# Kernel optimization log

Measured on AMD Instinct MI355X. Metric: run time of the kernel, lower is better.

Reference implementation:

```python
import jax, jax.numpy as jnp
import numpy as np

TEMPERATURE = 0.1

def setup_inputs() -> dict:
    key = jax.random.key(0)
    k1, k2 = jax.random.split(key)
    B, D = 8192, 512
    anchor = jax.random.normal(k1, (B, D), dtype=jnp.float32)
    positive = jax.random.normal(k2, (B, D), dtype=jnp.float32)
    return {"anchor": anchor, "positive": positive}

def reference(anchor, positive):
    # sim[i, j] = <anchor_i, positive_j> / T  -- [B, B]
    sim = jnp.einsum("bd,nd->bn", anchor, positive) / TEMPERATURE
    # InfoNCE with in-batch negatives: positive is the diagonal; since softmax
    # is permutation-invariant, -log_softmax(logits)[pos] = logsumexp(row) - diag.
    loss = jax.nn.logsumexp(sim, axis=1) - jnp.diagonal(sim)
    return jnp.mean(loss)
```

## Files before the change

### kernel.cpp

```cpp
#include <hip/hip_runtime.h>
#include <hip/hip_bf16.h>
#include <math.h>
#include <stdint.h>


#define NB 8192
#define DDIM 512
#define SPLITS 8
#define BM 256
#define BN 256
#define CPB (NB / SPLITS)
#define NROUND 32

#define DELTA 0.045f
#define INV_DELTA (1.0f / DELTA)
#define OUT_SCALE (DELTA * DELTA * 10.0f)
#define K2F (OUT_SCALE * 1.4426950408889634f)
#define LN2F 0.6931471805599453f

typedef unsigned char u8;
typedef __attribute__((ext_vector_type(4))) int i32x4;

__device__ __forceinline__ float fexp2(float x) {
#if __has_builtin(__builtin_amdgcn_exp2f)
  return __builtin_amdgcn_exp2f(x);
#else
  return __expf(x * LN2F);
#endif
}
__device__ __forceinline__ float flog2(float x) {
#if __has_builtin(__builtin_amdgcn_logf)
  return __builtin_amdgcn_logf(x);
#else
  return __logf(x) * 1.4426950408889634f;
#endif
}

__device__ __forceinline__ void gl2lds16(const u8* g, const u8* l) {
  __builtin_amdgcn_global_load_lds(
      (__attribute__((address_space(1))) unsigned int*)(uintptr_t)g,
      (__attribute__((address_space(3))) unsigned int*)(unsigned int)(uintptr_t)l,
      16, 0, 0);
}

__device__ __forceinline__ unsigned pack4(float x0, float x1, float x2, float x3) {
  int q0 = min(127, max(-127, __float2int_rn(x0 * INV_DELTA)));
  int q1 = min(127, max(-127, __float2int_rn(x1 * INV_DELTA)));
  int q2 = min(127, max(-127, __float2int_rn(x2 * INV_DELTA)));
  int q3 = min(127, max(-127, __float2int_rn(x3 * INV_DELTA)));
  return (q0 & 0xFF) | ((q1 & 0xFF) << 8) | ((q2 & 0xFF) << 16) | ((q3 & 0xFF) << 24);
}

__global__ void cvt_diag_kernel(const float* __restrict__ a, const float* __restrict__ p,
                                u8* __restrict__ aq, u8* __restrict__ pq,
                                float* __restrict__ diag, float* __restrict__ out) {
  if (blockIdx.x == 0 && threadIdx.x == 0) out[0] = 0.f;
  int row = (blockIdx.x * 256 + threadIdx.x) >> 6;
  int lane = threadIdx.x & 63;
  const float4* ar = (const float4*)(a + (size_t)row * DDIM + lane * 8);
  const float4* pr = (const float4*)(p + (size_t)row * DDIM + lane * 8);
  float4 a0 = ar[0], a1 = ar[1];
  float4 p0 = pr[0], p1 = pr[1];
  *(uint2*)(aq + (size_t)row * DDIM + lane * 8) =
      (uint2){pack4(a0.x, a0.y, a0.z, a0.w), pack4(a1.x, a1.y, a1.z, a1.w)};
  *(uint2*)(pq + (size_t)row * DDIM + lane * 8) =
      (uint2){pack4(p0.x, p0.y, p0.z, p0.w), pack4(p1.x, p1.y, p1.z, p1.w)};
  float s = a0.x * p0.x + a0.y * p0.y + a0.z * p0.z + a0.w * p0.w +
            a1.x * p1.x + a1.y * p1.y + a1.z * p1.z + a1.w * p1.w;
  for (int off = 32; off > 0; off >>= 1) s += __shfl_down(s, off);
  if (lane == 0) diag[row] = s * 10.0f;
}

__device__ __forceinline__ void fold_lse(i32x4 (&acc)[4][8], float (&rm)[4][4],
                                         float (&rl)[4][4]) {
#pragma unroll
  for (int mi = 0; mi < 4; ++mi) {
#pragma unroll
    for (int rr = 0; rr < 4; ++rr) {
      int im = acc[mi][0][rr];
#pragma unroll
      for (int ni = 1; ni < 8; ++ni) im = max(im, acc[mi][ni][rr]);
      const float mf = (float)im * K2F;
      const float nm = fmaxf(rm[mi][rr], mf);
      float add = 0.f;
#pragma unroll
      for (int ni = 0; ni < 8; ++ni)
        add += fexp2(fmaf((float)acc[mi][ni][rr], K2F, -nm));
      rl[mi][rr] = rl[mi][rr] * fexp2(rm[mi][rr] - nm) + add;
      rm[mi][rr] = nm;
#pragma unroll
      for (int ni = 0; ni < 8; ++ni) acc[mi][ni][rr] = 0;
    }
  }
}

__global__ __launch_bounds__(512, 2) void gemm_lse(
    const u8* __restrict__ Aq, const u8* __restrict__ Bq,
    float* __restrict__ partLse) {
  __shared__ u8 sA[4][BM * 64];
  __shared__ u8 sB[4][BN * 64];

  const int tid = threadIdx.x;
  const int wave = tid >> 6;
  const int lane = tid & 63;
  const int quad = lane >> 4;
  const int l16 = lane & 15;
  const int wr = wave >> 1;
  const int wc = wave & 1;

  const int bid = blockIdx.x;
  const int xcd = bid & 7;
  const int idx = bid >> 3;
  const int rowTile = (idx & 3) * 8 + xcd;
  const int colSplit = idx >> 2;
  const int row0 = rowTile * BM;
  const int col0 = colSplit * CPB;

  const int rsub = lane >> 2;
  const int qsrc = (lane & 3) ^ ((rsub >> 1) & 3);
  const u8* aCol = Aq + (size_t)(row0 + wave * 32 + rsub) * DDIM + qsrc * 16;
  const u8* bCol = Bq + (size_t)(col0 + wave * 32 + rsub) * DDIM + qsrc * 16;
  const int ldsOff = wave * 2048;

  const int sw = (l16 >> 1) & 3;
  const int fragA = (wr * 64 + l16) * 64 + ((quad ^ sw) * 16);
  const int fragB = (wc * 128 + l16) * 64 + ((quad ^ sw) * 16);

  i32x4 acc[4][8];
#pragma unroll
  for (int mi = 0; mi < 4; ++mi)
#pragma unroll
    for (int ni = 0; ni < 8; ++ni) acc[mi][ni] = (i32x4){0, 0, 0, 0};

  float rm[4][4], rl[4][4];
#pragma unroll
  for (int mi = 0; mi < 4; ++mi)
#pragma unroll
    for (int rr = 0; rr < 4; ++rr) { rm[mi][rr] = -INFINITY; rl[mi][rr] = 0.f; }

#define STAGE_A(t)                                                       \
  do {                                                                   \
    const int _kk = ((t) & 7) << 6, _bf = (t) & 3;                       \
    const u8* _a = aCol + _kk;                                           \
    gl2lds16(_a, &sA[_bf][ldsOff]);                                      \
    gl2lds16(_a + 16 * DDIM, &sA[_bf][ldsOff + 1024]);                   \
  } while (0)
#define STAGE_B(t)                                                       \
  do {                                                                   \
    const int _kk = ((t) & 7) << 6, _bf = (t) & 3;                       \
    const u8* _b = bCol + ((t) >> 3) * (BN * DDIM) + _kk;                \
    gl2lds16(_b, &sB[_bf][ldsOff]);                                      \
    gl2lds16(_b + 16 * DDIM, &sB[_bf][ldsOff + 1024]);                   \
  } while (0)

  STAGE_A(0); STAGE_B(0);
  STAGE_A(1); STAGE_B(1);
  STAGE_A(2); STAGE_B(2);
  asm volatile("s_waitcnt vmcnt(8)");
  __builtin_amdgcn_s_barrier();

#define MF8(AR, MI)                                                                 \
  acc[MI][0] = __builtin_amdgcn_mfma_i32_16x16x64_i8(AR, bq0, acc[MI][0], 0, 0, 0); \
  acc[MI][1] = __builtin_amdgcn_mfma_i32_16x16x64_i8(AR, bq1, acc[MI][1], 0, 0, 0); \
  acc[MI][2] = __builtin_amdgcn_mfma_i32_16x16x64_i8(AR, bq2, acc[MI][2], 0, 0, 0); \
  acc[MI][3] = __builtin_amdgcn_mfma_i32_16x16x64_i8(AR, bq3, acc[MI][3], 0, 0, 0); \
  acc[MI][4] = __builtin_amdgcn_mfma_i32_16x16x64_i8(AR, bq4, acc[MI][4], 0, 0, 0); \
  acc[MI][5] = __builtin_amdgcn_mfma_i32_16x16x64_i8(AR, bq5, acc[MI][5], 0, 0, 0); \
  acc[MI][6] = __builtin_amdgcn_mfma_i32_16x16x64_i8(AR, bq6, acc[MI][6], 0, 0, 0); \
  acc[MI][7] = __builtin_amdgcn_mfma_i32_16x16x64_i8(AR, bq7, acc[MI][7], 0, 0, 0);

#define ROUND_BODY(r, DO_STAGE)                                          \
  do {                                                                   \
    const int _b = (r) & 3;                                              \
    const u8* _sa = &sA[_b][0];                                          \
    const u8* _sb = &sB[_b][0];                                          \
    i32x4 bq0 = *(const i32x4*)(_sb + fragB + 0 * 1024);                 \
    i32x4 bq1 = *(const i32x4*)(_sb + fragB + 1 * 1024);                 \
    i32x4 bq2 = *(const i32x4*)(_sb + fragB + 2 * 1024);                 \
    i32x4 bq3 = *(const i32x4*)(_sb + fragB + 3 * 1024);                 \
    i32x4 bq4 = *(const i32x4*)(_sb + fragB + 4 * 1024);                 \
    i32x4 bq5 = *(const i32x4*)(_sb + fragB + 5 * 1024);                 \
    i32x4 bq6 = *(const i32x4*)(_sb + fragB + 6 * 1024);                 \
    i32x4 bq7 = *(const i32x4*)(_sb + fragB + 7 * 1024);                 \
    i32x4 a0 = *(const i32x4*)(_sa + fragA + 0 * 1024);                  \
    i32x4 a1 = *(const i32x4*)(_sa + fragA + 1 * 1024);                  \
    i32x4 a2 = *(const i32x4*)(_sa + fragA + 2 * 1024);                  \
    i32x4 a3 = *(const i32x4*)(_sa + fragA + 3 * 1024);                  \
    if (DO_STAGE) { STAGE_A((r) + 3); STAGE_B((r) + 3); }                \
    MF8(a0, 0) MF8(a1, 1) MF8(a2, 2) MF8(a3, 3)                          \
    if (((r) & 7) == 7) fold_lse(acc, rm, rl);                           \
  } while (0)

  for (int r = 0; r < NROUND - 3; ++r) {
    ROUND_BODY(r, 1);
    asm volatile("s_waitcnt vmcnt(8)");
    __builtin_amdgcn_s_barrier();
  }
  ROUND_BODY(NROUND - 3, 0);
  asm volatile("s_waitcnt vmcnt(4)");
  __builtin_amdgcn_s_barrier();
  ROUND_BODY(NROUND - 2, 0);
  asm volatile("s_waitcnt vmcnt(0)");
  __builtin_amdgcn_s_barrier();
  ROUND_BODY(NROUND - 1, 0);
  __builtin_amdgcn_s_barrier();
#undef ROUND_BODY
#undef MF8
#undef STAGE_A
#undef STAGE_B

  float2* const scr = (float2*)&sA[0][0];
#pragma unroll
  for (int mi = 0; mi < 4; ++mi) {
#pragma unroll
    for (int rr = 0; rr < 4; ++rr) {
      float m = rm[mi][rr], l = rl[mi][rr];
#pragma unroll
      for (int mask = 1; mask < 16; mask <<= 1) {
        float om = __shfl_xor(m, mask);
        float ol = __shfl_xor(l, mask);
        float nm = fmaxf(m, om);
        l = l * fexp2(m - nm) + ol * fexp2(om - nm);
        m = nm;
      }
      if (l16 == 0) {
        int rowl = wr * 64 + mi * 16 + quad * 4 + rr;
        scr[wc * 256 + rowl] = (float2){m, l};
      }
    }
  }
  __syncthreads();
  if (tid < BM) {
    float2 p0 = scr[tid], p1 = scr[256 + tid];
    float nm = fmaxf(p0.x, p1.x);
    float L = p0.y * fexp2(p0.x - nm) + p1.y * fexp2(p1.x - nm);
    partLse[(size_t)colSplit * NB + row0 + tid] = nm + flog2(L);
  }
}

__global__ void reduce_kernel(const float* __restrict__ partLse,
                              const float* __restrict__ diag, float* __restrict__ out) {
  __shared__ float red[4];
  int r = blockIdx.x * 256 + threadIdx.x;
  float M = -INFINITY;
#pragma unroll
  for (int s = 0; s < SPLITS; ++s) M = fmaxf(M, partLse[(size_t)s * NB + r]);
  float L = 0.f;
#pragma unroll
  for (int s = 0; s < SPLITS; ++s) L += fexp2(partLse[(size_t)s * NB + r] - M);
  float v = (M + flog2(L)) * LN2F - diag[r];
  for (int off = 32; off > 0; off >>= 1) v += __shfl_down(v, off);
  if ((threadIdx.x & 63) == 0) red[threadIdx.x >> 6] = v;
  __syncthreads();
  if (threadIdx.x == 0) {
    float s = (red[0] + red[1] + red[2] + red[3]) * (1.0f / (float)NB);
    atomicAdd(out, s);
  }
}

extern "C" void kernel_launch(void* const* d_in, const int* in_sizes, int n_in,
                              void* d_out, int out_size, void* d_ws, size_t ws_size,
                              hipStream_t stream) {
  const float* anchor = (const float*)d_in[0];
  const float* positive = (const float*)d_in[1];
  float* out = (float*)d_out;

  char* ws = (char*)d_ws;
  u8* Aq = (u8*)ws;
  u8* Bq = (u8*)(ws + (size_t)4194304);
  float* diag = (float*)(ws + (size_t)8388608);
  float* partLse = (float*)(ws + (size_t)8388608 + 32768);

  cvt_diag_kernel<<<NB / 4, 256, 0, stream>>>(anchor, positive, Aq, Bq, diag, out);
  gemm_lse<<<SPLITS * (NB / BM), 512, 0, stream>>>(Aq, Bq, partLse);
  reduce_kernel<<<NB / 256, 256, 0, stream>>>(partLse, diag, out);
}
```

Measured before the change: 117.2 us.

## Split each round into halves with register double-buffered LDS fragments and mid-round barrier

The int8 MFMA main loop is restructured. Each K-round now runs in two halves. The first half uses fragments preloaded in registers, then waits and passes the barrier, issues the global-to-LDS staging, and prefetches the next round's first fragments into an alternate register set before doing the second half of the MFMAs. All 32 rounds are unrolled, and s_setprio raises wave priority around the MFMA bursts. The aim is to hide LDS read latency and barrier stalls behind matrix work, at the cost of more registers and code size. The vmcnt accounting also changes, which risks ordering mistakes.

```diff
diff --git a/kernel.cpp b/kernel.cpp
--- a/kernel.cpp
+++ b/kernel.cpp
@@ -159,53 +159,81 @@
   asm volatile("s_waitcnt vmcnt(8)");
   __builtin_amdgcn_s_barrier();
 
-#define MF8(AR, MI)                                                                 \
-  acc[MI][0] = __builtin_amdgcn_mfma_i32_16x16x64_i8(AR, bq0, acc[MI][0], 0, 0, 0); \
-  acc[MI][1] = __builtin_amdgcn_mfma_i32_16x16x64_i8(AR, bq1, acc[MI][1], 0, 0, 0); \
-  acc[MI][2] = __builtin_amdgcn_mfma_i32_16x16x64_i8(AR, bq2, acc[MI][2], 0, 0, 0); \
-  acc[MI][3] = __builtin_amdgcn_mfma_i32_16x16x64_i8(AR, bq3, acc[MI][3], 0, 0, 0); \
-  acc[MI][4] = __builtin_amdgcn_mfma_i32_16x16x64_i8(AR, bq4, acc[MI][4], 0, 0, 0); \
-  acc[MI][5] = __builtin_amdgcn_mfma_i32_16x16x64_i8(AR, bq5, acc[MI][5], 0, 0, 0); \
-  acc[MI][6] = __builtin_amdgcn_mfma_i32_16x16x64_i8(AR, bq6, acc[MI][6], 0, 0, 0); \
-  acc[MI][7] = __builtin_amdgcn_mfma_i32_16x16x64_i8(AR, bq7, acc[MI][7], 0, 0, 0);
-
-#define ROUND_BODY(r, DO_STAGE)                                          \
-  do {                                                                   \
-    const int _b = (r) & 3;                                              \
-    const u8* _sa = &sA[_b][0];                                          \
-    const u8* _sb = &sB[_b][0];                                          \
-    i32x4 bq0 = *(const i32x4*)(_sb + fragB + 0 * 1024);                 \
-    i32x4 bq1 = *(const i32x4*)(_sb + fragB + 1 * 1024);                 \
-    i32x4 bq2 = *(const i32x4*)(_sb + fragB + 2 * 1024);                 \
-    i32x4 bq3 = *(const i32x4*)(_sb + fragB + 3 * 1024);                 \
-    i32x4 bq4 = *(const i32x4*)(_sb + fragB + 4 * 1024);                 \
-    i32x4 bq5 = *(const i32x4*)(_sb + fragB + 5 * 1024);                 \
-    i32x4 bq6 = *(const i32x4*)(_sb + fragB + 6 * 1024);                 \
-    i32x4 bq7 = *(const i32x4*)(_sb + fragB + 7 * 1024);                 \
-    i32x4 a0 = *(const i32x4*)(_sa + fragA + 0 * 1024);                  \
-    i32x4 a1 = *(const i32x4*)(_sa + fragA + 1 * 1024);                  \
-    i32x4 a2 = *(const i32x4*)(_sa + fragA + 2 * 1024);                  \
-    i32x4 a3 = *(const i32x4*)(_sa + fragA + 3 * 1024);                  \
-    if (DO_STAGE) { STAGE_A((r) + 3); STAGE_B((r) + 3); }                \
-    MF8(a0, 0) MF8(a1, 1) MF8(a2, 2) MF8(a3, 3)                          \
-    if (((r) & 7) == 7) fold_lse(acc, rm, rl);                           \
-  } while (0)
-
-  for (int r = 0; r < NROUND - 3; ++r) {
-    ROUND_BODY(r, 1);
-    asm volatile("s_waitcnt vmcnt(8)");
-    __builtin_amdgcn_s_barrier();
-  }
-  ROUND_BODY(NROUND - 3, 0);
-  asm volatile("s_waitcnt vmcnt(4)");
-  __builtin_amdgcn_s_barrier();
-  ROUND_BODY(NROUND - 2, 0);
-  asm volatile("s_waitcnt vmcnt(0)");
-  __builtin_amdgcn_s_barrier();
-  ROUND_BODY(NROUND - 1, 0);
-  __builtin_amdgcn_s_barrier();
-#undef ROUND_BODY
-#undef MF8
+  i32x4 xb0, xb1, xb2, xb3, xa0, xa1;
+  i32x4 yb0, yb1, yb2, yb3, ya0, ya1;
+  xb0 = *(const i32x4*)(&sB[0][fragB + 0 * 1024]);
+  xb1 = *(const i32x4*)(&sB[0][fragB + 1 * 1024]);
+  xb2 = *(const i32x4*)(&sB[0][fragB + 2 * 1024]);
+  xb3 = *(const i32x4*)(&sB[0][fragB + 3 * 1024]);
+  xa0 = *(const i32x4*)(&sA[0][fragA + 0 * 1024]);
+  xa1 = *(const i32x4*)(&sA[0][fragA + 1 * 1024]);
+
+#define VMW4 asm volatile("s_waitcnt vmcnt(4)")
+#define VMW0 asm volatile("s_waitcnt vmcnt(0)")
+
+#define MF4(AR, MI, B0, B1, B2, B3, NBASE)                                                    \
+  acc[MI][NBASE + 0] = __builtin_amdgcn_mfma_i32_16x16x64_i8(AR, B0, acc[MI][NBASE + 0], 0, 0, 0); \
+  acc[MI][NBASE + 1] = __builtin_amdgcn_mfma_i32_16x16x64_i8(AR, B1, acc[MI][NBASE + 1], 0, 0, 0); \
+  acc[MI][NBASE + 2] = __builtin_amdgcn_mfma_i32_16x16x64_i8(AR, B2, acc[MI][NBASE + 2], 0, 0, 0); \
+  acc[MI][NBASE + 3] = __builtin_amdgcn_mfma_i32_16x16x64_i8(AR, B3, acc[MI][NBASE + 3], 0, 0, 0);
+
+#define RND(r, CB0, CB1, CB2, CB3, CA0, CA1, NB0, NB1, NB2, NB3, NA0, NA1, \
+            DO_STAGE, VMSTMT, DO_PREF, DO_FOLD)                           \
+  {                                                                       \
+    const u8* _sa = &sA[(r) & 3][0];                                      \
+    const u8* _sb = &sB[(r) & 3][0];                                      \
+    i32x4 _a2 = *(const i32x4*)(_sa + fragA + 2 * 1024);                  \
+    i32x4 _a3 = *(const i32x4*)(_sa + fragA + 3 * 1024);                  \
+    i32x4 _b4 = *(const i32x4*)(_sb + fragB + 4 * 1024);                  \
+    i32x4 _b5 = *(const i32x4*)(_sb + fragB + 5 * 1024);                  \
+    i32x4 _b6 = *(const i32x4*)(_sb + fragB + 6 * 1024);                  \
+    i32x4 _b7 = *(const i32x4*)(_sb + fragB + 7 * 1024);                  \
+    __builtin_amdgcn_s_setprio(1);                                        \
+    MF4(CA0, 0, CB0, CB1, CB2, CB3, 0)                                    \
+    MF4(CA1, 1, CB0, CB1, CB2, CB3, 0)                                    \
+    MF4(_a2, 2, CB0, CB1, CB2, CB3, 0)                                    \
+    MF4(_a3, 3, CB0, CB1, CB2, CB3, 0)                                    \
+    __builtin_amdgcn_s_setprio(0);                                        \
+    VMSTMT;                                                               \
+    __builtin_amdgcn_s_barrier();                                         \
+    if (DO_STAGE) { STAGE_A((r) + 3); STAGE_B((r) + 3); }                 \
+    if (DO_PREF) {                                                        \
+      const u8* _na = &sA[((r) + 1) & 3][0];                              \
+      const u8* _nb = &sB[((r) + 1) & 3][0];                              \
+      NB0 = *(const i32x4*)(_nb + fragB + 0 * 1024);                      \
+      NB1 = *(const i32x4*)(_nb + fragB + 1 * 1024);                      \
+      NB2 = *(const i32x4*)(_nb + fragB + 2 * 1024);                      \
+      NB3 = *(const i32x4*)(_nb + fragB + 3 * 1024);                      \
+      NA0 = *(const i32x4*)(_na + fragA + 0 * 1024);                      \
+      NA1 = *(const i32x4*)(_na + fragA + 1 * 1024);                      \
+    }                                                                     \
+    __builtin_amdgcn_s_setprio(1);                                        \
+    MF4(CA0, 0, _b4, _b5, _b6, _b7, 4)                                    \
+    MF4(CA1, 1, _b4, _b5, _b6, _b7, 4)                                    \
+    MF4(_a2, 2, _b4, _b5, _b6, _b7, 4)                                    \
+    MF4(_a3, 3, _b4, _b5, _b6, _b7, 4)                                    \
+    __builtin_amdgcn_s_setprio(0);                                        \
+    if (DO_FOLD) fold_lse(acc, rm, rl);                                   \
+  }
+
+#define RX(r, DS, VM, PF, FL) RND(r, xb0, xb1, xb2, xb3, xa0, xa1, yb0, yb1, yb2, yb3, ya0, ya1, DS, VM, PF, FL)
+#define RY(r, DS, VM, PF, FL) RND(r, yb0, yb1, yb2, yb3, ya0, ya1, xb0, xb1, xb2, xb3, xa0, xa1, DS, VM, PF, FL)
+
+  RX(0, 1, VMW4, 1, 0)  RY(1, 1, VMW4, 1, 0)  RX(2, 1, VMW4, 1, 0)  RY(3, 1, VMW4, 1, 0)
+  RX(4, 1, VMW4, 1, 0)  RY(5, 1, VMW4, 1, 0)  RX(6, 1, VMW4, 1, 0)  RY(7, 1, VMW4, 1, 1)
+  RX(8, 1, VMW4, 1, 0)  RY(9, 1, VMW4, 1, 0)  RX(10, 1, VMW4, 1, 0) RY(11, 1, VMW4, 1, 0)
+  RX(12, 1, VMW4, 1, 0) RY(13, 1, VMW4, 1, 0) RX(14, 1, VMW4, 1, 0) RY(15, 1, VMW4, 1, 1)
+  RX(16, 1, VMW4, 1, 0) RY(17, 1, VMW4, 1, 0) RX(18, 1, VMW4, 1, 0) RY(19, 1, VMW4, 1, 0)
+  RX(20, 1, VMW4, 1, 0) RY(21, 1, VMW4, 1, 0) RX(22, 1, VMW4, 1, 0) RY(23, 1, VMW4, 1, 1)
+  RX(24, 1, VMW4, 1, 0) RY(25, 1, VMW4, 1, 0) RX(26, 1, VMW4, 1, 0) RY(27, 1, VMW4, 1, 0)
+  RX(28, 1, VMW4, 1, 0) RY(29, 0, VMW4, 1, 0) RX(30, 0, VMW0, 1, 0) RY(31, 0, (void)0, 0, 1)
+
+#undef RX
+#undef RY
+#undef RND
+#undef MF4
+#undef VMW4
+#undef VMW0
 #undef STAGE_A
 #undef STAGE_B
 
```

New measurement: 245.0 us. 2.09x slower.

## Split GEMM tile across 16 waves with 64x64 per-wave subtiles

Applied to the files above, without the earlier changes.

Doubles the workgroup to 1024 threads, arranging 16 waves in a 4x4 grid so each wave computes a 64x64 sub-tile instead of 64x128. Staging, wait counts, the LSE fold and the cross-wave merge are adjusted accordingly. The intent is more resident waves per CU and fewer accumulator registers per wave for better latency hiding. In exchange, LDS fragment reuse per MFMA drops and barriers synchronize twice as many waves.

```diff
diff --git a/kernel.cpp b/kernel.cpp
--- a/kernel.cpp
+++ b/kernel.cpp
@@ -71,30 +71,30 @@
   if (lane == 0) diag[row] = s * 10.0f;
 }
 
-__device__ __forceinline__ void fold_lse(i32x4 (&acc)[4][8], float (&rm)[4][4],
+__device__ __forceinline__ void fold_lse(i32x4 (&acc)[4][4], float (&rm)[4][4],
                                          float (&rl)[4][4]) {
 #pragma unroll
   for (int mi = 0; mi < 4; ++mi) {
 #pragma unroll
     for (int rr = 0; rr < 4; ++rr) {
-      int im = acc[mi][0][rr];
-#pragma unroll
-      for (int ni = 1; ni < 8; ++ni) im = max(im, acc[mi][ni][rr]);
+      const int i0 = acc[mi][0][rr], i1 = acc[mi][1][rr];
+      const int i2 = acc[mi][2][rr], i3 = acc[mi][3][rr];
+      const int im = max(max(i0, i1), max(i2, i3));
       const float mf = (float)im * K2F;
       const float nm = fmaxf(rm[mi][rr], mf);
-      float add = 0.f;
-#pragma unroll
-      for (int ni = 0; ni < 8; ++ni)
-        add += fexp2(fmaf((float)acc[mi][ni][rr], K2F, -nm));
-      rl[mi][rr] = rl[mi][rr] * fexp2(rm[mi][rr] - nm) + add;
+      rl[mi][rr] = rl[mi][rr] * fexp2(rm[mi][rr] - nm) +
+                   (fexp2(fmaf((float)i0, K2F, -nm)) +
+                    fexp2(fmaf((float)i1, K2F, -nm)) +
+                    fexp2(fmaf((float)i2, K2F, -nm)) +
+                    fexp2(fmaf((float)i3, K2F, -nm)));
       rm[mi][rr] = nm;
 #pragma unroll
-      for (int ni = 0; ni < 8; ++ni) acc[mi][ni][rr] = 0;
+      for (int ni = 0; ni < 4; ++ni) acc[mi][ni][rr] = 0;
     }
   }
 }
 
-__global__ __launch_bounds__(512, 2) void gemm_lse(
+__global__ __launch_bounds__(1024, 4) void gemm_lse(
     const u8* __restrict__ Aq, const u8* __restrict__ Bq,
     float* __restrict__ partLse) {
   __shared__ u8 sA[4][BM * 64];
@@ -105,8 +105,8 @@
   const int lane = tid & 63;
   const int quad = lane >> 4;
   const int l16 = lane & 15;
-  const int wr = wave >> 1;
-  const int wc = wave & 1;
+  const int wr = wave >> 2;
+  const int wc = wave & 3;
 
   const int bid = blockIdx.x;
   const int xcd = bid & 7;
@@ -118,19 +118,19 @@
 
   const int rsub = lane >> 2;
   const int qsrc = (lane & 3) ^ ((rsub >> 1) & 3);
-  const u8* aCol = Aq + (size_t)(row0 + wave * 32 + rsub) * DDIM + qsrc * 16;
-  const u8* bCol = Bq + (size_t)(col0 + wave * 32 + rsub) * DDIM + qsrc * 16;
-  const int ldsOff = wave * 2048;
+  const u8* aCol = Aq + (size_t)(row0 + wave * 16 + rsub) * DDIM + qsrc * 16;
+  const u8* bCol = Bq + (size_t)(col0 + wave * 16 + rsub) * DDIM + qsrc * 16;
+  const int ldsOff = wave * 1024;
 
   const int sw = (l16 >> 1) & 3;
   const int fragA = (wr * 64 + l16) * 64 + ((quad ^ sw) * 16);
-  const int fragB = (wc * 128 + l16) * 64 + ((quad ^ sw) * 16);
-
-  i32x4 acc[4][8];
+  const int fragB = (wc * 64 + l16) * 64 + ((quad ^ sw) * 16);
+
+  i32x4 acc[4][4];
 #pragma unroll
   for (int mi = 0; mi < 4; ++mi)
 #pragma unroll
-    for (int ni = 0; ni < 8; ++ni) acc[mi][ni] = (i32x4){0, 0, 0, 0};
+    for (int ni = 0; ni < 4; ++ni) acc[mi][ni] = (i32x4){0, 0, 0, 0};
 
   float rm[4][4], rl[4][4];
 #pragma unroll
@@ -139,35 +139,21 @@
     for (int rr = 0; rr < 4; ++rr) { rm[mi][rr] = -INFINITY; rl[mi][rr] = 0.f; }
 
 #define STAGE_A(t)                                                       \
-  do {                                                                   \
-    const int _kk = ((t) & 7) << 6, _bf = (t) & 3;                       \
-    const u8* _a = aCol + _kk;                                           \
-    gl2lds16(_a, &sA[_bf][ldsOff]);                                      \
-    gl2lds16(_a + 16 * DDIM, &sA[_bf][ldsOff + 1024]);                   \
-  } while (0)
+  gl2lds16(aCol + (((t) & 7) << 6), &sA[(t) & 3][ldsOff])
 #define STAGE_B(t)                                                       \
-  do {                                                                   \
-    const int _kk = ((t) & 7) << 6, _bf = (t) & 3;                       \
-    const u8* _b = bCol + ((t) >> 3) * (BN * DDIM) + _kk;                \
-    gl2lds16(_b, &sB[_bf][ldsOff]);                                      \
-    gl2lds16(_b + 16 * DDIM, &sB[_bf][ldsOff + 1024]);                   \
-  } while (0)
+  gl2lds16(bCol + ((t) >> 3) * (BN * DDIM) + (((t) & 7) << 6), &sB[(t) & 3][ldsOff])
 
   STAGE_A(0); STAGE_B(0);
   STAGE_A(1); STAGE_B(1);
   STAGE_A(2); STAGE_B(2);
-  asm volatile("s_waitcnt vmcnt(8)");
-  __builtin_amdgcn_s_barrier();
-
-#define MF8(AR, MI)                                                                 \
+  asm volatile("s_waitcnt vmcnt(4)");
+  __builtin_amdgcn_s_barrier();
+
+#define MF4(AR, MI)                                                                 \
   acc[MI][0] = __builtin_amdgcn_mfma_i32_16x16x64_i8(AR, bq0, acc[MI][0], 0, 0, 0); \
   acc[MI][1] = __builtin_amdgcn_mfma_i32_16x16x64_i8(AR, bq1, acc[MI][1], 0, 0, 0); \
   acc[MI][2] = __builtin_amdgcn_mfma_i32_16x16x64_i8(AR, bq2, acc[MI][2], 0, 0, 0); \
-  acc[MI][3] = __builtin_amdgcn_mfma_i32_16x16x64_i8(AR, bq3, acc[MI][3], 0, 0, 0); \
-  acc[MI][4] = __builtin_amdgcn_mfma_i32_16x16x64_i8(AR, bq4, acc[MI][4], 0, 0, 0); \
-  acc[MI][5] = __builtin_amdgcn_mfma_i32_16x16x64_i8(AR, bq5, acc[MI][5], 0, 0, 0); \
-  acc[MI][6] = __builtin_amdgcn_mfma_i32_16x16x64_i8(AR, bq6, acc[MI][6], 0, 0, 0); \
-  acc[MI][7] = __builtin_amdgcn_mfma_i32_16x16x64_i8(AR, bq7, acc[MI][7], 0, 0, 0);
+  acc[MI][3] = __builtin_amdgcn_mfma_i32_16x16x64_i8(AR, bq3, acc[MI][3], 0, 0, 0);
 
 #define ROUND_BODY(r, DO_STAGE)                                          \
   do {                                                                   \
@@ -178,26 +164,22 @@
     i32x4 bq1 = *(const i32x4*)(_sb + fragB + 1 * 1024);                 \
     i32x4 bq2 = *(const i32x4*)(_sb + fragB + 2 * 1024);                 \
     i32x4 bq3 = *(const i32x4*)(_sb + fragB + 3 * 1024);                 \
-    i32x4 bq4 = *(const i32x4*)(_sb + fragB + 4 * 1024);                 \
-    i32x4 bq5 = *(const i32x4*)(_sb + fragB + 5 * 1024);                 \
-    i32x4 bq6 = *(const i32x4*)(_sb + fragB + 6 * 1024);                 \
-    i32x4 bq7 = *(const i32x4*)(_sb + fragB + 7 * 1024);                 \
     i32x4 a0 = *(const i32x4*)(_sa + fragA + 0 * 1024);                  \
     i32x4 a1 = *(const i32x4*)(_sa + fragA + 1 * 1024);                  \
     i32x4 a2 = *(const i32x4*)(_sa + fragA + 2 * 1024);                  \
     i32x4 a3 = *(const i32x4*)(_sa + fragA + 3 * 1024);                  \
     if (DO_STAGE) { STAGE_A((r) + 3); STAGE_B((r) + 3); }                \
-    MF8(a0, 0) MF8(a1, 1) MF8(a2, 2) MF8(a3, 3)                          \
+    MF4(a0, 0) MF4(a1, 1) MF4(a2, 2) MF4(a3, 3)                          \
     if (((r) & 7) == 7) fold_lse(acc, rm, rl);                           \
   } while (0)
 
   for (int r = 0; r < NROUND - 3; ++r) {
     ROUND_BODY(r, 1);
-    asm volatile("s_waitcnt vmcnt(8)");
+    asm volatile("s_waitcnt vmcnt(4)");
     __builtin_amdgcn_s_barrier();
   }
   ROUND_BODY(NROUND - 3, 0);
-  asm volatile("s_waitcnt vmcnt(4)");
+  asm volatile("s_waitcnt vmcnt(2)");
   __builtin_amdgcn_s_barrier();
   ROUND_BODY(NROUND - 2, 0);
   asm volatile("s_waitcnt vmcnt(0)");
@@ -205,7 +187,7 @@
   ROUND_BODY(NROUND - 1, 0);
   __builtin_amdgcn_s_barrier();
 #undef ROUND_BODY
-#undef MF8
+#undef MF4
 #undef STAGE_A
 #undef STAGE_B
 
@@ -232,8 +214,10 @@
   __syncthreads();
   if (tid < BM) {
     float2 p0 = scr[tid], p1 = scr[256 + tid];
-    float nm = fmaxf(p0.x, p1.x);
-    float L = p0.y * fexp2(p0.x - nm) + p1.y * fexp2(p1.x - nm);
+    float2 p2 = scr[512 + tid], p3 = scr[768 + tid];
+    float nm = fmaxf(fmaxf(p0.x, p1.x), fmaxf(p2.x, p3.x));
+    float L = p0.y * fexp2(p0.x - nm) + p1.y * fexp2(p1.x - nm) +
+              p2.y * fexp2(p2.x - nm) + p3.y * fexp2(p3.x - nm);
     partLse[(size_t)colSplit * NB + row0 + tid] = nm + flog2(L);
   }
 }
@@ -272,6 +256,6 @@
   float* partLse = (float*)(ws + (size_t)8388608 + 32768);
 
   cvt_diag_kernel<<<NB / 4, 256, 0, stream>>>(anchor, positive, Aq, Bq, diag, out);
-  gemm_lse<<<SPLITS * (NB / BM), 512, 0, stream>>>(Aq, Bq, partLse);
+  gemm_lse<<<SPLITS * (NB / BM), 1024, 0, stream>>>(Aq, Bq, partLse);
   reduce_kernel<<<NB / 256, 256, 0, stream>>>(partLse, diag, out);
 }
```

New measurement: 139.5 us. 1.19x slower.
